# Performance work log

Hardware: AMD Instinct MI355X
Metric: run time of the kernel (lower is better)

## Reference

```python
import jax, jax.numpy as jnp
import numpy as np

GROUPS = 8
EPS = 1e-3  # keras GroupNormalization default epsilon


def group_norm(x, gamma, beta):
    # Keras GroupNormalization(axis=-1): reduce over all non-batch, non-group axes.
    B, L, C = x.shape
    xg = x.reshape(B, L, GROUPS, C // GROUPS)
    mean = jnp.mean(xg, axis=(1, 3), keepdims=True)          # [B,1,G,1]
    var = jnp.var(xg, axis=(1, 3), keepdims=True)
    xn = ((xg - mean) * jax.lax.rsqrt(var + EPS)).reshape(B, L, C)
    return xn * gamma + beta


def setup_inputs() -> dict:
    key = jax.random.key(0)
    ks = jax.random.split(key, 6)
    B, L, C = 8, 2048, 512
    x = jax.random.normal(ks[0], (B, L, C), dtype=jnp.float32)
    s = 0.02
    return {
        "x": x,
        "gamma": jnp.ones((C,), jnp.float32),
        "beta": jnp.zeros((C,), jnp.float32),
        "wq": jax.random.normal(ks[1], (C, C), jnp.float32) * s,
        "bq": jnp.zeros((C,), jnp.float32),
        "wk": jax.random.normal(ks[2], (C, C), jnp.float32) * s,
        "bk": jnp.zeros((C,), jnp.float32),
        "wv": jax.random.normal(ks[3], (C, C), jnp.float32) * s,
        "bv": jnp.zeros((C,), jnp.float32),
        "wp": jax.random.normal(ks[4], (C, C), jnp.float32) * s,
        "bp": jnp.zeros((C,), jnp.float32),
    }


def reference(x, gamma, beta, wq, bq, wk, bk, wv, bv, wp, bp):
    C = x.shape[-1]
    scale = jnp.float32(C) ** -0.5
    h = group_norm(x, gamma, beta)                           # normalized input (also residual!)
    q = h @ wq + bq                                          # [B,L,C]
    k = h @ wk + bk
    v = h @ wv + bv
    attn = jnp.einsum('blc,bLc->blL', q, k) * scale          # [B,L,L]
    attn = jax.nn.softmax(attn, axis=-1)
    o = jnp.einsum('blL,bLc->blc', attn, v)                  # [B,L,C]
    o = o @ wp + bp
    return h + o
```

## Files before the change

kernel.cpp:

```cpp
#include <hip/hip_runtime.h>
#include <hip/hip_bf16.h>
#include <cstdint>

typedef unsigned short ushort_t;
typedef __bf16  bf16x8 __attribute__((ext_vector_type(8)));
typedef float   f32x4  __attribute__((ext_vector_type(4)));

#define L_SEQ 2048
#define C_DIM 512
#define B_SZ  8
#define N_GROUPS 8
#define CG 64

__device__ __forceinline__ float bf2f(ushort_t u) {
    union { uint32_t i; float f; } x; x.i = ((uint32_t)u) << 16; return x.f;
}
__device__ __forceinline__ ushort_t f2bf(float f) {
    union { float f; uint32_t i; } x; x.f = f;
    uint32_t i = x.i;
    uint32_t r = (i + 0x7FFFu + ((i >> 16) & 1u)) >> 16;
    return (ushort_t)r;
}

__device__ __forceinline__ void gl_lds16(const ushort_t* g, ushort_t* l) {
    __builtin_amdgcn_global_load_lds(
        (const __attribute__((address_space(1))) unsigned int*)g,
        (__attribute__((address_space(3))) unsigned int*)l, 16, 0, 0);
}

__global__ __launch_bounds__(256) void conv_wT(const float* __restrict__ wq,
                                               const float* __restrict__ wk,
                                               const float* __restrict__ wv,
                                               const float* __restrict__ wp,
                                               ushort_t* __restrict__ wqkvT,
                                               ushort_t* __restrict__ wpT) {
    __shared__ ushort_t Ts[64][72];
    int blk = blockIdx.x, tid = threadIdx.x;
    int mat = blk >> 6, t = blk & 63;
    int k0 = (t >> 3) * 64, n0 = (t & 7) * 64;
    const float* srcs[4] = {wq, wk, wv, wp};
    const float* src = srcs[mat];
    #pragma unroll
    for (int i = 0; i < 2; ++i) {
        int idx = tid * 2 + i;
        int row = idx >> 3, c8 = (idx & 7) * 8;
        const float* p = src + (size_t)(k0 + row) * 512 + n0 + c8;
        float4 a = *(const float4*)p;
        float4 b = *(const float4*)(p + 4);
        Ts[row][c8 + 0] = f2bf(a.x); Ts[row][c8 + 1] = f2bf(a.y);
        Ts[row][c8 + 2] = f2bf(a.z); Ts[row][c8 + 3] = f2bf(a.w);
        Ts[row][c8 + 4] = f2bf(b.x); Ts[row][c8 + 5] = f2bf(b.y);
        Ts[row][c8 + 6] = f2bf(b.z); Ts[row][c8 + 7] = f2bf(b.w);
    }
    __syncthreads();
    int dr = tid >> 2, lc = (tid & 3) * 16;
    union { uint4 v[2]; ushort_t u[16]; } o;
    #pragma unroll
    for (int j = 0; j < 16; ++j) o.u[j] = Ts[lc + j][dr];
    ushort_t* dst = (mat == 3 ? wpT + (size_t)(n0 + dr) * 512
                              : wqkvT + (size_t)(mat * 512 + n0 + dr) * 512) + k0 + lc;
    *(uint4*)dst = o.v[0];
    *(uint4*)(dst + 8) = o.v[1];
}

__global__ __launch_bounds__(256) void gn_stats(const float* __restrict__ x,
                                                float* __restrict__ sums) {
    int bg = blockIdx.x >> 3, sp = blockIdx.x & 7;
    int b = bg >> 3, g = bg & 7;
    int tid = threadIdx.x;
    const float* base = x + ((size_t)b * L_SEQ + sp * 256) * C_DIM + g * CG;
    float s = 0.f, s2 = 0.f;
    #pragma unroll
    for (int it = 0; it < 8; ++it) {
        int i = it * 2048 + tid * 8;
        int l = i >> 6, c = i & 63;
        const float* p = base + (size_t)l * C_DIM + c;
        float4 a = *(const float4*)p;
        float4 bb = *(const float4*)(p + 4);
        s  += a.x + a.y + a.z + a.w + bb.x + bb.y + bb.z + bb.w;
        s2 += a.x*a.x + a.y*a.y + a.z*a.z + a.w*a.w
            + bb.x*bb.x + bb.y*bb.y + bb.z*bb.z + bb.w*bb.w;
    }
    #pragma unroll
    for (int off = 32; off > 0; off >>= 1) { s += __shfl_down(s, off); s2 += __shfl_down(s2, off); }
    __shared__ float rs[4], rs2[4];
    int wave = tid >> 6;
    if ((tid & 63) == 0) { rs[wave] = s; rs2[wave] = s2; }
    __syncthreads();
    if (tid == 0) {
        sums[bg * 16 + sp * 2 + 0] = rs[0] + rs[1] + rs[2] + rs[3];
        sums[bg * 16 + sp * 2 + 1] = rs2[0] + rs2[1] + rs2[2] + rs2[3];
    }
}

__global__ __launch_bounds__(256) void gn_apply(const float* __restrict__ x,
                                                const float* __restrict__ gamma,
                                                const float* __restrict__ beta,
                                                const float* __restrict__ sums,
                                                ushort_t* __restrict__ h) {
    size_t e = ((size_t)blockIdx.x * 256 + threadIdx.x) * 8;
    int c = (int)(e % C_DIM);
    size_t bl = e / C_DIM;
    int b = (int)(bl / L_SEQ);
    int g = c >> 6;
    int bg = b * 8 + g;
    float s = 0.f, s2 = 0.f;
    #pragma unroll
    for (int sp = 0; sp < 8; ++sp) { s += sums[bg * 16 + sp * 2]; s2 += sums[bg * 16 + sp * 2 + 1]; }
    const float N = (float)(L_SEQ * CG);
    float mean = s / N;
    float var  = s2 / N - mean * mean;
    float rstd = rsqrtf(var + 1e-3f);
    float4 a = *(const float4*)(x + e);
    float4 bb = *(const float4*)(x + e + 4);
    float xf[8] = {a.x, a.y, a.z, a.w, bb.x, bb.y, bb.z, bb.w};
    union { uint4 v; ushort_t u[8]; } o;
    #pragma unroll
    for (int i = 0; i < 8; ++i)
        o.u[i] = f2bf((xf[i] - mean) * rstd * gamma[c + i] + beta[c + i]);
    *(uint4*)(h + e) = o.v;
}

template<bool PROJ>
__global__ __launch_bounds__(256) void gemm128(const ushort_t* __restrict__ A,
                                               const ushort_t* __restrict__ BT,
                                               const float* __restrict__ b0,
                                               const float* __restrict__ b1,
                                               const float* __restrict__ b2,
                                               const ushort_t* __restrict__ res,
                                               ushort_t* __restrict__ o0,
                                               ushort_t* __restrict__ o1,
                                               ushort_t* __restrict__ o2,
                                               float* __restrict__ of) {
    __shared__ ushort_t As[128][32];
    __shared__ ushort_t Bs[128][32];
    int tid = threadIdx.x, lane = tid & 63, w = tid >> 6;
    int l15 = lane & 15, quad = lane >> 4;
    int m0 = blockIdx.y * 128;
    int n0g = blockIdx.x * 128;
    int wm = w >> 1, wn = w & 1;
    int lr = lane >> 2, lc = (lane & 3) * 8;
    f32x4 acc[4][4] = {};
    for (int k0 = 0; k0 < 512; k0 += 32) {
        #pragma unroll
        for (int j = 0; j < 2; ++j) {
            int rb = (w * 2 + j) * 16;
            gl_lds16(A  + (size_t)(m0 + rb + lr) * 512 + k0 + lc, &As[rb][0]);
            gl_lds16(BT + (size_t)(n0g + rb + lr) * 512 + k0 + lc, &Bs[rb][0]);
        }
        __syncthreads();
        bf16x8 af[4], bf[4];
        #pragma unroll
        for (int t = 0; t < 4; ++t) {
            af[t] = *(const bf16x8*)&As[wm * 64 + t * 16 + l15][quad * 8];
            bf[t] = *(const bf16x8*)&Bs[wn * 64 + t * 16 + l15][quad * 8];
        }
        #pragma unroll
        for (int mt = 0; mt < 4; ++mt)
            #pragma unroll
            for (int nt = 0; nt < 4; ++nt)
                acc[mt][nt] = __builtin_amdgcn_mfma_f32_16x16x32_bf16(af[mt], bf[nt], acc[mt][nt], 0, 0, 0);
        __syncthreads();
    }
    int seg = n0g >> 9;
    const float* bias = PROJ ? b0 : (seg == 0 ? b0 : (seg == 1 ? b1 : b2));
    ushort_t* ob = PROJ ? (ushort_t*)nullptr : (seg == 0 ? o0 : (seg == 1 ? o1 : o2));
    int ns = n0g & 511;
    #pragma unroll
    for (int mt = 0; mt < 4; ++mt)
        #pragma unroll
        for (int nt = 0; nt < 4; ++nt) {
            int n = ns + wn * 64 + nt * 16 + l15;
            float bv = bias[n];
            #pragma unroll
            for (int r = 0; r < 4; ++r) {
                int m = m0 + wm * 64 + mt * 16 + quad * 4 + r;
                float v = acc[mt][nt][r] + bv;
                if (PROJ) of[(size_t)m * 512 + n] = v + bf2f(res[(size_t)m * 512 + n]);
                else      ob[(size_t)m * 512 + n] = f2bf(v);
            }
        }
}

__global__ __launch_bounds__(256) void transpose_v(const ushort_t* __restrict__ V,
                                                   ushort_t* __restrict__ vT) {
    __shared__ ushort_t Ts[64][72];
    int tid = threadIdx.x;
    int l0 = blockIdx.x * 64, d0 = blockIdx.y * 64, b = blockIdx.z;
    const ushort_t* Vb = V + (size_t)b * L_SEQ * C_DIM;
    #pragma unroll
    for (int i = 0; i < 2; ++i) {
        int idx = tid * 2 + i;
        int row = idx >> 3, c8 = (idx & 7) * 8;
        *(uint4*)&Ts[row][c8] = *(const uint4*)(Vb + (size_t)(l0 + row) * 512 + d0 + c8);
    }
    __syncthreads();
    int dr = tid >> 2, lc = (tid & 3) * 16;
    union { uint4 v[2]; ushort_t u[16]; } o;
    #pragma unroll
    for (int j = 0; j < 16; ++j) o.u[j] = Ts[lc + j][dr];
    ushort_t* dst = vT + ((size_t)b * C_DIM + d0 + dr) * L_SEQ + l0 + lc;
    *(uint4*)dst = o.v[0];
    *(uint4*)(dst + 8) = o.v[1];
}

__global__ __launch_bounds__(768, 3) void attn6(const ushort_t* __restrict__ Q,
                                                const ushort_t* __restrict__ K,
                                                const ushort_t* __restrict__ vT,
                                                ushort_t* __restrict__ O) {
    __shared__ ushort_t Ks[2][32][520];
    __shared__ ushort_t Vs[2][512][32];
    __shared__ ushort_t Ps[2][64][40];
    __shared__ float    Al[2][64];
    __shared__ float    Lb[64];
    int tid = threadIdx.x;
    int lane = tid & 63, w = tid >> 6;
    int l15 = lane & 15, quad = lane >> 4;
    int b  = blockIdx.x & 7;
    int qt = blockIdx.x >> 3;
    const float scale2 = 0.044194173824159216f * 1.4426950408889634f;
    const ushort_t* Qb = Q + (size_t)b * L_SEQ * C_DIM;
    const ushort_t* Kb = K + (size_t)b * L_SEQ * C_DIM;
    const ushort_t* Vt = vT + (size_t)b * C_DIM * L_SEQ;
    ushort_t* Ob = O + (size_t)b * L_SEQ * C_DIM;

    bool isQK = (w < 4);
    int pw = w - 4;
    int d0 = pw * 64;

    bf16x8 qf[16];
    float m_r = -1e30f, l_r = 0.f;
    f32x4 acc[4][4];

    if (isQK) {
        int qr = qt * 64 + w * 16 + l15;
        #pragma unroll
        for (int ks = 0; ks < 16; ++ks)
            qf[ks] = *(const bf16x8*)(Qb + (size_t)qr * C_DIM + ks * 32 + quad * 8);
    } else {
        #pragma unroll
        for (int qi = 0; qi < 4; ++qi)
            #pragma unroll
            for (int nt = 0; nt < 4; ++nt) acc[qi][nt] = (f32x4){0.f, 0.f, 0.f, 0.f};
        #pragma unroll
        for (int i = 0; i < 4; ++i) {
            int row = pw * 4 + i;
            gl_lds16(Kb + (size_t)row * C_DIM + lane * 8, &Ks[0][row][0]);
        }
    }
    __syncthreads();

    for (int kt = 0; kt <= 64; ++kt) {
        int cur = kt & 1, prv = cur ^ 1;
        if (isQK) {
            if (kt < 64) {
                f32x4 s0 = (f32x4){0.f, 0.f, 0.f, 0.f};
                f32x4 s1 = (f32x4){0.f, 0.f, 0.f, 0.f};
                __builtin_amdgcn_s_setprio(1);
                #pragma unroll
                for (int ks = 0; ks < 16; ++ks) {
                    bf16x8 kf0 = *(const bf16x8*)&Ks[cur][l15][ks * 32 + quad * 8];
                    bf16x8 kf1 = *(const bf16x8*)&Ks[cur][16 + l15][ks * 32 + quad * 8];
                    s0 = __builtin_amdgcn_mfma_f32_16x16x32_bf16(kf0, qf[ks], s0, 0, 0, 0);
                    s1 = __builtin_amdgcn_mfma_f32_16x16x32_bf16(kf1, qf[ks], s1, 0, 0, 0);
                }
                __builtin_amdgcn_s_setprio(0);
                float mx = fmaxf(fmaxf(fmaxf(s0[0], s0[1]), fmaxf(s0[2], s0[3])),
                                 fmaxf(fmaxf(s1[0], s1[1]), fmaxf(s1[2], s1[3])));
                mx = fmaxf(mx, __shfl_xor(mx, 16, 64));
                mx = fmaxf(mx, __shfl_xor(mx, 32, 64));
                mx *= scale2;
                float mn = fmaxf(m_r, mx);
                float alpha = exp2f(m_r - mn);
                m_r = mn;
                ushort_t pb[8];
                float rs = 0.f;
                #pragma unroll
                for (int r = 0; r < 4; ++r) {
                    pb[r]     = f2bf(exp2f(s0[r] * scale2 - mn));
                    pb[4 + r] = f2bf(exp2f(s1[r] * scale2 - mn));
                    rs += bf2f(pb[r]) + bf2f(pb[4 + r]);
                }
                rs += __shfl_xor(rs, 16, 64);
                rs += __shfl_xor(rs, 32, 64);
                l_r = l_r * alpha + rs;
                int row = w * 16 + l15;
                uint2 w0, w1;
                w0.x = (uint32_t)pb[0] | ((uint32_t)pb[1] << 16);
                w0.y = (uint32_t)pb[2] | ((uint32_t)pb[3] << 16);
                w1.x = (uint32_t)pb[4] | ((uint32_t)pb[5] << 16);
                w1.y = (uint32_t)pb[6] | ((uint32_t)pb[7] << 16);
                *(uint2*)&Ps[cur][row][quad * 4] = w0;
                *(uint2*)&Ps[cur][row][16 + quad * 4] = w1;
                if (lane < 16) Al[cur][w * 16 + lane] = alpha;
            } else {
                if (lane < 16) Lb[w * 16 + lane] = l_r;
            }
        } else {
            if (kt < 63) {
                #pragma unroll
                for (int i = 0; i < 4; ++i) {
                    int row = pw * 4 + i;
                    gl_lds16(Kb + (size_t)((kt + 1) * 32 + row) * C_DIM + lane * 8, &Ks[prv][row][0]);
                }
            }
            if (kt < 64) {
                int k0 = kt * 32;
                #pragma unroll
                for (int i = 0; i < 4; ++i) {
                    int r0 = (pw * 4 + i) * 16;
                    gl_lds16(Vt + (size_t)(r0 + (lane >> 2)) * L_SEQ + k0 + (lane & 3) * 8,
                             &Vs[cur][r0][0]);
                }
            }
            if (kt > 0) {
                bf16x8 pf[4];
                #pragma unroll
                for (int qi = 0; qi < 4; ++qi)
                    pf[qi] = *(const bf16x8*)&Ps[prv][qi * 16 + l15][quad * 8];
                #pragma unroll
                for (int qi = 0; qi < 4; ++qi) {
                    float4 av = *(const float4*)&Al[prv][qi * 16 + quad * 4];
                    #pragma unroll
                    for (int nt = 0; nt < 4; ++nt) {
                        acc[qi][nt][0] *= av.x; acc[qi][nt][1] *= av.y;
                        acc[qi][nt][2] *= av.z; acc[qi][nt][3] *= av.w;
                    }
                }
                bf16x8 vf[4];
                #pragma unroll
                for (int nt = 0; nt < 4; ++nt)
                    vf[nt] = *(const bf16x8*)&Vs[prv][d0 + nt * 16 + l15][quad * 8];
                __builtin_amdgcn_s_setprio(1);
                #pragma unroll
                for (int nt = 0; nt < 4; ++nt)
                    #pragma unroll
                    for (int qi = 0; qi < 4; ++qi)
                        acc[qi][nt] = __builtin_amdgcn_mfma_f32_16x16x32_bf16(pf[qi], vf[nt], acc[qi][nt], 0, 0, 0);
                __builtin_amdgcn_s_setprio(0);
            }
        }
        __syncthreads();
    }
    if (!isQK) {
        #pragma unroll
        for (int qi = 0; qi < 4; ++qi) {
            float4 lv = *(const float4*)&Lb[qi * 16 + quad * 4];
            float inv[4] = {1.f / lv.x, 1.f / lv.y, 1.f / lv.z, 1.f / lv.w};
            #pragma unroll
            for (int r = 0; r < 4; ++r) {
                int m = qt * 64 + qi * 16 + quad * 4 + r;
                #pragma unroll
                for (int nt = 0; nt < 4; ++nt)
                    Ob[(size_t)m * 512 + d0 + nt * 16 + l15] = f2bf(acc[qi][nt][r] * inv[r]);
            }
        }
    }
}

extern "C" void kernel_launch(void* const* d_in, const int* in_sizes, int n_in,
                              void* d_out, int out_size, void* d_ws, size_t ws_size,
                              hipStream_t stream) {
    const float* x     = (const float*)d_in[0];
    const float* gamma = (const float*)d_in[1];
    const float* beta  = (const float*)d_in[2];
    const float* wq    = (const float*)d_in[3];
    const float* bq    = (const float*)d_in[4];
    const float* wk    = (const float*)d_in[5];
    const float* bk    = (const float*)d_in[6];
    const float* wv    = (const float*)d_in[7];
    const float* bv    = (const float*)d_in[8];
    const float* wp    = (const float*)d_in[9];
    const float* bp    = (const float*)d_in[10];
    float* out = (float*)d_out;

    const size_t MC = (size_t)B_SZ * L_SEQ * C_DIM;
    const size_t WC = (size_t)C_DIM * C_DIM;
    ushort_t* h     = (ushort_t*)d_ws;
    ushort_t* qb    = h     + MC;
    ushort_t* kb    = qb    + MC;
    ushort_t* vbuf  = kb    + MC;
    ushort_t* vtb   = vbuf  + MC;
    ushort_t* wqkvT = vtb   + MC;
    ushort_t* wpT   = wqkvT + 3 * WC;
    float* sums     = (float*)(wpT + WC);

    conv_wT<<<dim3(256), dim3(256), 0, stream>>>(wq, wk, wv, wp, wqkvT, wpT);
    gn_stats<<<dim3(512), dim3(256), 0, stream>>>(x, sums);
    gn_apply<<<dim3(4096), dim3(256), 0, stream>>>(x, gamma, beta, sums, h);

    gemm128<false><<<dim3(12, 128), dim3(256), 0, stream>>>(h, wqkvT, bq, bk, bv, nullptr,
                                                            qb, kb, vbuf, nullptr);

    transpose_v<<<dim3(32, 8, 8), dim3(256), 0, stream>>>(vbuf, vtb);

    attn6<<<dim3(256), dim3(768), 0, stream>>>(qb, kb, vtb, vbuf);

    gemm128<true><<<dim3(4, 128), dim3(256), 0, stream>>>(vbuf, wpT, bp, nullptr, nullptr, h,
                                                          nullptr, nullptr, nullptr, out);
}
```

Measured before the change: 326.4 us.

## Compute V transposed directly via swapped GEMM, widen K tile with swizzled LDS

The V projection now runs as a separate GEMM with the operands swapped (Wv^T times h^T), so its output lands directly in the transposed [B,C,L] layout. This removes the standalone transpose kernel and its extra global round-trip. The GEMM K-step grows from 32 to 64 with an XOR-swizzled LDS layout, which halves the barrier count and is meant to avoid bank conflicts. The attention QK loop splits each accumulator into two independent chains so consecutive MFMAs do not depend on each other. The costs are an extra launch for the V GEMM and strided output stores in its epilogue.

```diff
diff --git a/kernel.cpp b/kernel.cpp
--- a/kernel.cpp
+++ b/kernel.cpp
@@ -121,93 +121,79 @@
     *(uint4*)(h + e) = o.v;
 }
 
-template<bool PROJ>
+template<int MODE>
 __global__ __launch_bounds__(256) void gemm128(const ushort_t* __restrict__ A,
                                                const ushort_t* __restrict__ BT,
                                                const float* __restrict__ b0,
                                                const float* __restrict__ b1,
-                                               const float* __restrict__ b2,
                                                const ushort_t* __restrict__ res,
                                                ushort_t* __restrict__ o0,
                                                ushort_t* __restrict__ o1,
-                                               ushort_t* __restrict__ o2,
                                                float* __restrict__ of) {
-    __shared__ ushort_t As[128][32];
-    __shared__ ushort_t Bs[128][32];
+    __shared__ ushort_t As[128][64];
+    __shared__ ushort_t Bs[128][64];
     int tid = threadIdx.x, lane = tid & 63, w = tid >> 6;
     int l15 = lane & 15, quad = lane >> 4;
     int m0 = blockIdx.y * 128;
     int n0g = blockIdx.x * 128;
     int wm = w >> 1, wn = w & 1;
-    int lr = lane >> 2, lc = (lane & 3) * 8;
+    int lr8 = lane >> 3;
+    int gch = (lane & 7) ^ lr8;
+    int h8  = l15 & 7;
     f32x4 acc[4][4] = {};
-    for (int k0 = 0; k0 < 512; k0 += 32) {
-        #pragma unroll
-        for (int j = 0; j < 2; ++j) {
-            int rb = (w * 2 + j) * 16;
-            gl_lds16(A  + (size_t)(m0 + rb + lr) * 512 + k0 + lc, &As[rb][0]);
-            gl_lds16(BT + (size_t)(n0g + rb + lr) * 512 + k0 + lc, &Bs[rb][0]);
+    for (int k0 = 0; k0 < 512; k0 += 64) {
+        #pragma unroll
+        for (int j = 0; j < 4; ++j) {
+            int rb = w * 32 + j * 8;
+            int r  = rb + lr8;
+            gl_lds16(A  + (size_t)(m0 + r) * 512 + k0 + gch * 8, &As[rb][0]);
+            gl_lds16(BT + (size_t)(n0g + r) * 512 + k0 + gch * 8, &Bs[rb][0]);
         }
         __syncthreads();
-        bf16x8 af[4], bf[4];
-        #pragma unroll
-        for (int t = 0; t < 4; ++t) {
-            af[t] = *(const bf16x8*)&As[wm * 64 + t * 16 + l15][quad * 8];
-            bf[t] = *(const bf16x8*)&Bs[wn * 64 + t * 16 + l15][quad * 8];
-        }
-        #pragma unroll
-        for (int mt = 0; mt < 4; ++mt)
-            #pragma unroll
-            for (int nt = 0; nt < 4; ++nt)
-                acc[mt][nt] = __builtin_amdgcn_mfma_f32_16x16x32_bf16(af[mt], bf[nt], acc[mt][nt], 0, 0, 0);
+        #pragma unroll
+        for (int kk = 0; kk < 2; ++kk) {
+            int slot = ((quad + 4 * kk) ^ h8) * 8;
+            bf16x8 af[4], bf[4];
+            #pragma unroll
+            for (int t = 0; t < 4; ++t) {
+                af[t] = *(const bf16x8*)&As[wm * 64 + t * 16 + l15][slot];
+                bf[t] = *(const bf16x8*)&Bs[wn * 64 + t * 16 + l15][slot];
+            }
+            #pragma unroll
+            for (int mt = 0; mt < 4; ++mt)
+                #pragma unroll
+                for (int nt = 0; nt < 4; ++nt)
+                    acc[mt][nt] = __builtin_amdgcn_mfma_f32_16x16x32_bf16(af[mt], bf[nt], acc[mt][nt], 0, 0, 0);
+        }
         __syncthreads();
     }
-    int seg = n0g >> 9;
-    const float* bias = PROJ ? b0 : (seg == 0 ? b0 : (seg == 1 ? b1 : b2));
-    ushort_t* ob = PROJ ? (ushort_t*)nullptr : (seg == 0 ? o0 : (seg == 1 ? o1 : o2));
-    int ns = n0g & 511;
     #pragma unroll
     for (int mt = 0; mt < 4; ++mt)
         #pragma unroll
         for (int nt = 0; nt < 4; ++nt) {
-            int n = ns + wn * 64 + nt * 16 + l15;
-            float bv = bias[n];
+            int n = (MODE == 0 ? (n0g & 511) : n0g) + wn * 64 + nt * 16 + l15;
+            float bvn = (MODE == 2) ? 0.f : (MODE == 1 ? b0[n] : (n0g >> 9 ? b1[n] : b0[n]));
             #pragma unroll
             for (int r = 0; r < 4; ++r) {
                 int m = m0 + wm * 64 + mt * 16 + quad * 4 + r;
-                float v = acc[mt][nt][r] + bv;
-                if (PROJ) of[(size_t)m * 512 + n] = v + bf2f(res[(size_t)m * 512 + n]);
-                else      ob[(size_t)m * 512 + n] = f2bf(v);
-            }
-        }
-}
-
-__global__ __launch_bounds__(256) void transpose_v(const ushort_t* __restrict__ V,
-                                                   ushort_t* __restrict__ vT) {
-    __shared__ ushort_t Ts[64][72];
-    int tid = threadIdx.x;
-    int l0 = blockIdx.x * 64, d0 = blockIdx.y * 64, b = blockIdx.z;
-    const ushort_t* Vb = V + (size_t)b * L_SEQ * C_DIM;
-    #pragma unroll
-    for (int i = 0; i < 2; ++i) {
-        int idx = tid * 2 + i;
-        int row = idx >> 3, c8 = (idx & 7) * 8;
-        *(uint4*)&Ts[row][c8] = *(const uint4*)(Vb + (size_t)(l0 + row) * 512 + d0 + c8);
-    }
-    __syncthreads();
-    int dr = tid >> 2, lc = (tid & 3) * 16;
-    union { uint4 v[2]; ushort_t u[16]; } o;
-    #pragma unroll
-    for (int j = 0; j < 16; ++j) o.u[j] = Ts[lc + j][dr];
-    ushort_t* dst = vT + ((size_t)b * C_DIM + d0 + dr) * L_SEQ + l0 + lc;
-    *(uint4*)dst = o.v[0];
-    *(uint4*)(dst + 8) = o.v[1];
-}
-
-__global__ __launch_bounds__(768, 3) void attn6(const ushort_t* __restrict__ Q,
-                                                const ushort_t* __restrict__ K,
-                                                const ushort_t* __restrict__ vT,
-                                                ushort_t* __restrict__ O) {
+                float v = acc[mt][nt][r];
+                if (MODE == 2) {
+                    v += b0[m];
+                    o0[(size_t)(n >> 11) * 1048576 + (size_t)m * 2048 + (n & 2047)] = f2bf(v);
+                } else if (MODE == 1) {
+                    of[(size_t)m * 512 + n] = v + bvn + bf2f(res[(size_t)m * 512 + n]);
+                } else {
+                    ushort_t* ob = (n0g >> 9) ? o1 : o0;
+                    ob[(size_t)m * 512 + n] = f2bf(v + bvn);
+                }
+            }
+        }
+}
+
+__global__ __launch_bounds__(768, 3) void attn11(const ushort_t* __restrict__ Q,
+                                                 const ushort_t* __restrict__ K,
+                                                 const ushort_t* __restrict__ vT,
+                                                 ushort_t* __restrict__ O) {
     __shared__ ushort_t Ks[2][32][520];
     __shared__ ushort_t Vs[2][512][32];
     __shared__ ushort_t Ps[2][64][40];
@@ -254,17 +240,25 @@
         int cur = kt & 1, prv = cur ^ 1;
         if (isQK) {
             if (kt < 64) {
-                f32x4 s0 = (f32x4){0.f, 0.f, 0.f, 0.f};
-                f32x4 s1 = (f32x4){0.f, 0.f, 0.f, 0.f};
+                f32x4 s0a = (f32x4){0.f, 0.f, 0.f, 0.f};
+                f32x4 s0b = (f32x4){0.f, 0.f, 0.f, 0.f};
+                f32x4 s1a = (f32x4){0.f, 0.f, 0.f, 0.f};
+                f32x4 s1b = (f32x4){0.f, 0.f, 0.f, 0.f};
                 __builtin_amdgcn_s_setprio(1);
                 #pragma unroll
-                for (int ks = 0; ks < 16; ++ks) {
+                for (int ks = 0; ks < 16; ks += 2) {
                     bf16x8 kf0 = *(const bf16x8*)&Ks[cur][l15][ks * 32 + quad * 8];
                     bf16x8 kf1 = *(const bf16x8*)&Ks[cur][16 + l15][ks * 32 + quad * 8];
-                    s0 = __builtin_amdgcn_mfma_f32_16x16x32_bf16(kf0, qf[ks], s0, 0, 0, 0);
-                    s1 = __builtin_amdgcn_mfma_f32_16x16x32_bf16(kf1, qf[ks], s1, 0, 0, 0);
+                    bf16x8 kf2 = *(const bf16x8*)&Ks[cur][l15][(ks + 1) * 32 + quad * 8];
+                    bf16x8 kf3 = *(const bf16x8*)&Ks[cur][16 + l15][(ks + 1) * 32 + quad * 8];
+                    s0a = __builtin_amdgcn_mfma_f32_16x16x32_bf16(kf0, qf[ks], s0a, 0, 0, 0);
+                    s1a = __builtin_amdgcn_mfma_f32_16x16x32_bf16(kf1, qf[ks], s1a, 0, 0, 0);
+                    s0b = __builtin_amdgcn_mfma_f32_16x16x32_bf16(kf2, qf[ks + 1], s0b, 0, 0, 0);
+                    s1b = __builtin_amdgcn_mfma_f32_16x16x32_bf16(kf3, qf[ks + 1], s1b, 0, 0, 0);
                 }
                 __builtin_amdgcn_s_setprio(0);
+                f32x4 s0 = s0a + s0b;
+                f32x4 s1 = s1a + s1b;
                 float mx = fmaxf(fmaxf(fmaxf(s0[0], s0[1]), fmaxf(s0[2], s0[3])),
                                  fmaxf(fmaxf(s1[0], s1[1]), fmaxf(s1[2], s1[3])));
                 mx = fmaxf(mx, __shfl_xor(mx, 16, 64));
@@ -389,13 +383,13 @@
     gn_stats<<<dim3(512), dim3(256), 0, stream>>>(x, sums);
     gn_apply<<<dim3(4096), dim3(256), 0, stream>>>(x, gamma, beta, sums, h);
 
-    gemm128<false><<<dim3(12, 128), dim3(256), 0, stream>>>(h, wqkvT, bq, bk, bv, nullptr,
-                                                            qb, kb, vbuf, nullptr);
-
-    transpose_v<<<dim3(32, 8, 8), dim3(256), 0, stream>>>(vbuf, vtb);
-
-    attn6<<<dim3(256), dim3(768), 0, stream>>>(qb, kb, vtb, vbuf);
-
-    gemm128<true><<<dim3(4, 128), dim3(256), 0, stream>>>(vbuf, wpT, bp, nullptr, nullptr, h,
-                                                          nullptr, nullptr, nullptr, out);
-}
+    gemm128<0><<<dim3(8, 128), dim3(256), 0, stream>>>(h, wqkvT, bq, bk, nullptr,
+                                                       qb, kb, nullptr);
+    gemm128<2><<<dim3(128, 4), dim3(256), 0, stream>>>(wqkvT + 2 * WC, h, bv, nullptr, nullptr,
+                                                       vtb, nullptr, nullptr);
+
+    attn11<<<dim3(256), dim3(768), 0, stream>>>(qb, kb, vtb, vbuf);
+
+    gemm128<1><<<dim3(4, 128), dim3(256), 0, stream>>>(vbuf, wpT, bp, nullptr, h,
+                                                       nullptr, nullptr, out);
+}
```

After: 319.8 us. 2.0% less time.
